# Kernel optimization log

Hardware: AMD Instinct MI355X
Metric: run time of the kernel (lower is better)

## Reference

```python
import jax, jax.numpy as jnp
import numpy as np

D_MODEL = 768
NUM_HEADS = 12
D_HEAD = D_MODEL // NUM_HEADS
LN_EPS = 1e-5


def layer_norm(x, w, b):
    m = jnp.mean(x, axis=-1, keepdims=True)
    v = jnp.mean(jnp.square(x - m), axis=-1, keepdims=True)
    return (x - m) * jax.lax.rsqrt(v + LN_EPS) * w + b


def setup_inputs() -> dict:
    key = jax.random.key(0)
    ks = jax.random.split(key, 10)
    B, P, NQ, D = 16, 197, 8, D_MODEL
    s = 1.0 / np.sqrt(D)
    return {
        "q_x": jax.random.normal(ks[0], (1, NQ, D), jnp.float32),
        "kv_x": jax.random.normal(ks[1], (B, P, D), jnp.float32),
        "pair_pos_embedding": jax.random.normal(ks[2], (2 * P, D), jnp.float32) * 0.02,
        "q_w": jax.random.normal(ks[3], (D, D), jnp.float32) * s,
        "q_b": jnp.zeros((D,), jnp.float32),
        "kv_w": jax.random.normal(ks[4], (D, D), jnp.float32) * s,
        "kv_b": jnp.zeros((D,), jnp.float32),
        "out_w": jax.random.normal(ks[5], (D, D), jnp.float32) * s,
        "out_b": jnp.zeros((D,), jnp.float32),
        "lnq_w": jnp.ones((D,), jnp.float32),
        "lnq_b": jnp.zeros((D,), jnp.float32),
        "lnkv_w": jnp.ones((D,), jnp.float32),
        "lnkv_b": jnp.zeros((D,), jnp.float32),
    }


def reference(q_x, kv_x, pair_pos_embedding, q_w, q_b, kv_w, kv_b,
              out_w, out_b, lnq_w, lnq_b, lnkv_w, lnkv_b):
    H, dh = NUM_HEADS, D_HEAD
    scale = dh ** -0.5
    _, NQ, D = q_x.shape
    B, P, _ = kv_x.shape

    # q path: Linear -> LN -> split heads -> [1, H, NQ, dh]
    q = layer_norm(q_x @ q_w.T + q_b, lnq_w, lnq_b)
    q = q.reshape(1, NQ, H, dh).transpose(0, 2, 1, 3)  # [1,H,NQ,dh]

    # kv path: Linear -> LN -> split heads -> [B, H, P, dh]
    kv = layer_norm(kv_x @ kv_w.T + kv_b, lnkv_w, lnkv_b)
    kv = kv.reshape(B, P, H, dh).transpose(0, 2, 1, 3)  # [B,H,P,dh]

    # pairwise expansion: kv_concat[i*B+j] = cat(kv[i], kv[j]) along token dim
    kv_rep = jnp.repeat(kv, B, axis=0)          # [B^2,H,P,dh] (repeat_interleave)
    kv_til = jnp.tile(kv, (B, 1, 1, 1))         # [B^2,H,P,dh]
    kv_cat = jnp.concatenate([kv_rep, kv_til], axis=2)  # [B^2,H,2P,dh]

    # positional bias: [2P, D] -> [1, H, 2P, dh]
    pos = pair_pos_embedding.reshape(1, 2 * P, H, dh).transpose(0, 2, 1, 3)
    kv_cat = kv_cat + pos

    scores = jnp.einsum('bhqd,bhpd->bhqp', jnp.broadcast_to(q, (B * B, H, NQ, dh)), kv_cat) * scale
    attn = jax.nn.softmax(scores, axis=-1)      # [B^2,H,NQ,2P]

    v1 = jnp.einsum('bhqp,bhpd->bhqd', attn[..., :P], kv_cat[:, :, :P, :])
    v2 = jnp.einsum('bhqp,bhpd->bhqd', attn[..., P:], kv_cat[:, :, P:, :])
    values = (v1 - v2).transpose(0, 2, 1, 3).reshape(B * B, NQ, D)
    return values @ out_w.T + out_b
```

## Files before the change

kernel.cpp:

```cpp
#include <hip/hip_runtime.h>
#include <hip/hip_bf16.h>
#include <math.h>

#define D_MODEL 768
#define NHEADS  12
#define DHEAD   64
#define NQR     8
#define BB      16
#define PP      197
#define NPAIR   256
#define MKV     (BB*PP)
#define LN_EPSF 1e-5f
#define SCALEF  0.125f

#define KTOT  2304
#define KSPLIT 3
#define KPER  (KTOT/KSPLIT)
#define MPAD  3200
#define BM 128
#define BN 128
#define BK 64

#define CH0   100
#define CH1   97
#define CHMAX 100

typedef __attribute__((ext_vector_type(8))) short short8v;
typedef __attribute__((ext_vector_type(4))) float float4v;

__device__ __forceinline__ void gload16(const void* g, void* l){
  __builtin_amdgcn_global_load_lds(
      (const __attribute__((address_space(1))) unsigned int*)g,
      (__attribute__((address_space(3))) unsigned int*)l, 16, 0, 0);
}

__device__ __forceinline__ float lane_bcast(float v, int src){
  return __int_as_float(__builtin_amdgcn_readlane(__float_as_int(v), src));
}

__global__ __launch_bounds__(192) void prep_kernel(
    const float* __restrict__ kvx, const float* __restrict__ kvw,
    __hip_bfloat16* __restrict__ Ab, __hip_bfloat16* __restrict__ Wb,
    const float* __restrict__ qx, const float* __restrict__ qw,
    float* __restrict__ qy)
{
  __shared__ float xs[NQR*D_MODEL];
  int b = blockIdx.x, t = threadIdx.x;
  if (b < MPAD + D_MODEL){
    const float* X; __hip_bfloat16* Y; int valid, mode, m;
    if (b < MPAD){ X = kvx; Y = Ab; valid = MKV;     mode = 0; m = b; }
    else         { X = kvw; Y = Wb; valid = D_MODEL; mode = 1; m = b - MPAD; }
    int k = t*4;
    float4 v = (m < valid) ? *(const float4*)&X[(size_t)m*D_MODEL + k]
                           : make_float4(0.f,0.f,0.f,0.f);
    float xsv[4] = {v.x, v.y, v.z, v.w};
    unsigned short hu[4], lu[4];
    #pragma unroll
    for (int i = 0; i < 4; i++){
      __hip_bfloat16 h = __float2bfloat16(xsv[i]);
      float hf = __bfloat162float(h);
      __hip_bfloat16 l = __float2bfloat16(xsv[i] - hf);
      hu[i] = *(unsigned short*)&h;
      lu[i] = *(unsigned short*)&l;
    }
    ushort4 hv = {hu[0], hu[1], hu[2], hu[3]};
    ushort4 lv = {lu[0], lu[1], lu[2], lu[3]};
    ushort4* row = (ushort4*)(Y + (size_t)m*KTOT);
    int s = k >> 2;
    if (mode == 0){ row[s] = hv; row[s+192] = hv; row[s+384] = lv; }
    else          { row[s] = hv; row[s+192] = lv; row[s+384] = hv; }
    return;
  }
  int b2 = b - (MPAD + D_MODEL);
  for (int e = t*4; e < NQR*D_MODEL; e += 768)
    *(float4*)&xs[e] = *(const float4*)&qx[e];
  __syncthreads();
  int col = t >> 5, lane = t & 31;
  int c = b2*6 + col;
  const float* wr = qw + (size_t)c*D_MODEL;
  float acc[NQR] = {};
  for (int k = lane*4; k < D_MODEL; k += 128){
    float4 w4 = *(const float4*)&wr[k];
    #pragma unroll
    for (int q = 0; q < NQR; q++){
      float4 x4 = *(const float4*)&xs[q*D_MODEL + k];
      acc[q] += x4.x*w4.x + x4.y*w4.y + x4.z*w4.z + x4.w*w4.w;
    }
  }
  #pragma unroll
  for (int q = 0; q < NQR; q++){
    float a = acc[q];
    for (int off = 16; off >= 1; off >>= 1) a += __shfl_xor(a, off, 32);
    if (lane == 0) qy[q*D_MODEL + c] = a;
  }
}

__global__ __launch_bounds__(256) void gemm_mfma_kernel(
    const __hip_bfloat16* __restrict__ Ab, const __hip_bfloat16* __restrict__ Wb,
    float* __restrict__ Cp)
{
  __shared__ __hip_bfloat16 As[BM*BK];
  __shared__ __hip_bfloat16 Bs[BN*BK];
  int tid = threadIdx.x;
  int wave = tid >> 6, lane = tid & 63;
  int m0 = blockIdx.x*BM, n0 = blockIdx.y*BN, kt = blockIdx.z;
  int wr = wave >> 1, wc = wave & 1;

  float4v acc[4][4];
  #pragma unroll
  for (int i = 0; i < 4; i++)
    #pragma unroll
    for (int j = 0; j < 4; j++)
      acc[i][j] = (float4v){0.f, 0.f, 0.f, 0.f};

  int sbase = wave*256;
  for (int st = 0; st < KPER/BK; ++st){
    int k0 = kt*KPER + st*BK;
    __syncthreads();
    #pragma unroll
    for (int i = 0; i < 4; i++){
      int s  = sbase + i*64 + lane;
      int r  = s >> 3, kg = s & 7;
      int kgg = kg ^ (r & 7);
      gload16(Ab + (size_t)(m0 + r)*KTOT + k0 + kgg*8, (char*)As + (size_t)s*16);
      gload16(Wb + (size_t)(n0 + r)*KTOT + k0 + kgg*8, (char*)Bs + (size_t)s*16);
    }
    __syncthreads();
    #pragma unroll
    for (int ks = 0; ks < 2; ks++){
      int kq = ks*4 + (lane >> 4);
      short8v af[4], bf[4];
      #pragma unroll
      for (int t = 0; t < 4; t++){
        int ar = wr*64 + t*16 + (lane & 15);
        int as_ = ar*8 + (kq ^ (ar & 7));
        af[t] = *(const short8v*)((const char*)As + (size_t)as_*16);
        int br = wc*64 + t*16 + (lane & 15);
        int bs_ = br*8 + (kq ^ (br & 7));
        bf[t] = *(const short8v*)((const char*)Bs + (size_t)bs_*16);
      }
      #pragma unroll
      for (int i = 0; i < 4; i++)
        #pragma unroll
        for (int j = 0; j < 4; j++)
          acc[i][j] = __builtin_amdgcn_mfma_f32_16x16x32_bf16(af[i], bf[j], acc[i][j], 0, 0, 0);
    }
  }

  float* C = Cp + (size_t)kt*MKV*D_MODEL;
  #pragma unroll
  for (int i = 0; i < 4; i++){
    int mb = m0 + wr*64 + i*16 + ((lane >> 4) << 2);
    #pragma unroll
    for (int j = 0; j < 4; j++){
      int n = n0 + wc*64 + j*16 + (lane & 15);
      #pragma unroll
      for (int r = 0; r < 4; r++){
        int m = mb + r;
        if (m < MKV) C[(size_t)m*D_MODEL + n] = acc[i][j][r];
      }
    }
  }
}

__global__ __launch_bounds__(256) void ln_all_kernel(
    const float* __restrict__ C0, const float* __restrict__ C1,
    const float* __restrict__ C2, const float* __restrict__ kv_b,
    const float* __restrict__ lnkv_w, const float* __restrict__ lnkv_b,
    float* __restrict__ kv_ln,
    const float* __restrict__ q_y, const float* __restrict__ q_b,
    const float* __restrict__ lnq_w, const float* __restrict__ lnq_b,
    float* __restrict__ q_ln)
{
  __shared__ float red[256], red2[256];
  int b = blockIdx.x, tid = threadIdx.x;
  const float *xa, *xb, *xc, *bias, *lw, *lb; float* outp; bool three;
  if (b < MKV){
    xa = C0 + (size_t)b*D_MODEL; xb = C1 + (size_t)b*D_MODEL;
    xc = C2 + (size_t)b*D_MODEL;
    bias = kv_b; lw = lnkv_w; lb = lnkv_b;
    outp = kv_ln + (size_t)b*D_MODEL; three = true;
  } else {
    int r = b - MKV;
    xa = q_y + (size_t)r*D_MODEL; xb = xa; xc = xa;
    bias = q_b; lw = lnq_w; lb = lnq_b;
    outp = q_ln + (size_t)r*D_MODEL; three = false;
  }
  float x0 = xa[tid      ] + (three ? xb[tid      ] + xc[tid      ] : 0.f) + bias[tid      ];
  float x1 = xa[tid + 256] + (three ? xb[tid + 256] + xc[tid + 256] : 0.f) + bias[tid + 256];
  float x2 = xa[tid + 512] + (three ? xb[tid + 512] + xc[tid + 512] : 0.f) + bias[tid + 512];
  red[tid] = x0 + x1 + x2; red2[tid] = x0*x0 + x1*x1 + x2*x2;
  __syncthreads();
  for (int st = 128; st > 0; st >>= 1){
    if (tid < st){ red[tid] += red[tid+st]; red2[tid] += red2[tid+st]; }
    __syncthreads();
  }
  float mean = red[0]*(1.f/768.f);
  float var  = red2[0]*(1.f/768.f) - mean*mean;
  float inv  = rsqrtf(var + LN_EPSF);
  outp[tid      ] = (x0-mean)*inv*lw[tid      ] + lb[tid      ];
  outp[tid + 256] = (x1-mean)*inv*lw[tid + 256] + lb[tid + 256];
  outp[tid + 512] = (x2-mean)*inv*lw[tid + 512] + lb[tid + 512];
}

__global__ __launch_bounds__(256) void rank_proj_kernel(
    const float* __restrict__ kv_ln, const float* __restrict__ q_ln,
    const float* __restrict__ ppe, const float* __restrict__ ow,
    float* __restrict__ z1O, float* __restrict__ z2O,
    float* __restrict__ p1, float* __restrict__ p2)
{
  __shared__ float A[CHMAX*65];
  __shared__ float Us[NQR*64];
  int r = blockIdx.x, h = blockIdx.y, half = blockIdx.z;
  int tid = threadIdx.x;
  int wave = tid >> 6, lane = tid & 63;
  int qa = 2*wave, qb = qa + 1;
  const float* qrowA = q_ln + (size_t)qa*D_MODEL + h*64;
  const float* qrowB = q_ln + (size_t)qb*D_MODEL + h*64;

  float ua = 0.f, ub = 0.f;
  float za = 0.f, zb = 0.f;

  for (int c = 0; c < 2; c++){
    int p0 = c ? CH0 : 0;
    int np = c ? CH1 : CH0;
    __syncthreads();
    for (int e = tid; e < np*16; e += 256){
      int p = e >> 4, dq = (e & 15) << 2;
      float4 a = *(const float4*)&kv_ln[((size_t)(r*PP + p0 + p))*D_MODEL + h*64 + dq];
      float4 b = *(const float4*)&ppe[((size_t)(half*PP + p0 + p))*D_MODEL + h*64 + dq];
      float* rw = &A[p*65 + dq];
      rw[0] = a.x + b.x; rw[1] = a.y + b.y;
      rw[2] = a.z + b.z; rw[3] = a.w + b.w;
    }
    __syncthreads();

    int p1v = lane + 64;
    bool v1 = p1v < np;
    int p1c = v1 ? p1v : 0;
    float s0a = 0.f, s0b = 0.f, s1a = 0.f, s1b = 0.f;
    for (int d = 0; d < 64; d++){
      float qva = qrowA[d];
      float qvb = qrowB[d];
      float a0 = A[lane*65 + d];
      float a1 = A[p1c*65 + d];
      s0a += qva*a0; s1a += qva*a1;
      s0b += qvb*a0; s1b += qvb*a1;
    }
    float e0a = __expf(s0a*SCALEF);
    float e0b = __expf(s0b*SCALEF);
    float e1a = v1 ? __expf(s1a*SCALEF) : 0.f;
    float e1b = v1 ? __expf(s1b*SCALEF) : 0.f;
    za += e0a + e1a;
    zb += e0b + e1b;

    for (int p = 0; p < 64; p++){
      float av = A[p*65 + lane];
      ua += lane_bcast(e0a, p) * av;
      ub += lane_bcast(e0b, p) * av;
    }
    for (int p = 64; p < np; p++){
      float av = A[p*65 + lane];
      ua += lane_bcast(e1a, p - 64) * av;
      ub += lane_bcast(e1b, p - 64) * av;
    }
  }

  for (int off = 32; off >= 1; off >>= 1){
    za += __shfl_xor(za, off);
    zb += __shfl_xor(zb, off);
  }
  float* zO = half ? z2O : z1O;
  if (lane == 0){
    zO[(r*NHEADS + h)*NQR + qa] = za;
    zO[(r*NHEADS + h)*NQR + qb] = zb;
  }
  Us[qa*64 + lane] = ua;
  Us[qb*64 + lane] = ub;
  __syncthreads();

  float acc[NQR][3];
  #pragma unroll
  for (int m = 0; m < NQR; m++){ acc[m][0]=0.f; acc[m][1]=0.f; acc[m][2]=0.f; }
  const float* owh = ow + h*64;
  for (int d4 = 0; d4 < 64; d4 += 4){
    float4 w0 = *(const float4*)&owh[(size_t)(tid      )*D_MODEL + d4];
    float4 w1 = *(const float4*)&owh[(size_t)(tid + 256)*D_MODEL + d4];
    float4 w2 = *(const float4*)&owh[(size_t)(tid + 512)*D_MODEL + d4];
    #pragma unroll
    for (int m = 0; m < NQR; m++){
      float4 u = *(const float4*)&Us[m*64 + d4];
      acc[m][0] += u.x*w0.x + u.y*w0.y + u.z*w0.z + u.w*w0.w;
      acc[m][1] += u.x*w1.x + u.y*w1.y + u.z*w1.z + u.w*w1.w;
      acc[m][2] += u.x*w2.x + u.y*w2.y + u.z*w2.z + u.w*w2.w;
    }
  }
  float* P = half ? p2 : p1;
  #pragma unroll
  for (int m = 0; m < NQR; m++){
    size_t obase = (((size_t)r*NHEADS + h)*NQR + m)*D_MODEL;
    #pragma unroll
    for (int j = 0; j < 3; j++)
      P[obase + tid + 256*j] = acc[m][j];
  }
}

__global__ __launch_bounds__(192) void combine_out_kernel(
    const float* __restrict__ z1, const float* __restrict__ z2,
    const float* __restrict__ p1, const float* __restrict__ p2,
    const float* __restrict__ out_b, float* __restrict__ out)
{
  __shared__ float cs[4][NHEADS];
  int i = blockIdx.x, q = blockIdx.y, jq = blockIdx.z;
  int j0 = jq*4;
  int tid = threadIdx.x;
  if (tid < 4*NHEADS){
    int j = tid / NHEADS, h = tid % NHEADS;
    int ii = (i*NHEADS + h)*NQR + q;
    int jj = ((j0 + j)*NHEADS + h)*NQR + q;
    cs[j][h] = 1.f / (z1[ii] + z2[jj]);
  }
  __syncthreads();

  int n4 = tid*4;
  float4 bv = *(const float4*)&out_b[n4];
  float4 acc[4];
  #pragma unroll
  for (int j = 0; j < 4; j++) acc[j] = bv;

  #pragma unroll
  for (int h = 0; h < NHEADS; h++){
    float4 a = *(const float4*)&p1[(((size_t)i*NHEADS + h)*NQR + q)*D_MODEL + n4];
    #pragma unroll
    for (int j = 0; j < 4; j++){
      float4 b = *(const float4*)&p2[(((size_t)(j0+j)*NHEADS + h)*NQR + q)*D_MODEL + n4];
      float c = cs[j][h];
      acc[j].x += c*(a.x - b.x);
      acc[j].y += c*(a.y - b.y);
      acc[j].z += c*(a.z - b.z);
      acc[j].w += c*(a.w - b.w);
    }
  }
  #pragma unroll
  for (int j = 0; j < 4; j++){
    int pair = i*BB + j0 + j;
    *(float4*)&out[((size_t)(pair*NQR + q))*D_MODEL + n4] = acc[j];
  }
}

extern "C" void kernel_launch(void* const* d_in, const int* in_sizes, int n_in,
                              void* d_out, int out_size, void* d_ws, size_t ws_size,
                              hipStream_t stream)
{
  const float* q_x    = (const float*)d_in[0];
  const float* kv_x   = (const float*)d_in[1];
  const float* ppe    = (const float*)d_in[2];
  const float* q_w    = (const float*)d_in[3];
  const float* q_b    = (const float*)d_in[4];
  const float* kv_w   = (const float*)d_in[5];
  const float* kv_b   = (const float*)d_in[6];
  const float* out_w  = (const float*)d_in[7];
  const float* out_b  = (const float*)d_in[8];
  const float* lnq_w  = (const float*)d_in[9];
  const float* lnq_b  = (const float*)d_in[10];
  const float* lnkv_w = (const float*)d_in[11];
  const float* lnkv_b = (const float*)d_in[12];
  float* out = (float*)d_out;

  float* ws    = (float*)d_ws;
  float* q_y   = ws;
  float* q_ln  = q_y  + NQR*D_MODEL;
  float* Abuf_f = q_ln + NQR*D_MODEL;
  float* Wbuf_f = Abuf_f + (size_t)MPAD*KTOT/2;
  float* C0    = Wbuf_f + (size_t)D_MODEL*KTOT/2;
  float* C1    = C0 + (size_t)MKV*D_MODEL;
  float* C2    = C1 + (size_t)MKV*D_MODEL;

  __hip_bfloat16* Abuf = (__hip_bfloat16*)Abuf_f;
  __hip_bfloat16* Wbuf = (__hip_bfloat16*)Wbuf_f;

  float* kv_ln = Abuf_f;
  float* z1    = Wbuf_f;
  float* z2    = z1 + BB*NHEADS*NQR;
  float* p1    = C0;
  float* p2    = p1 + (size_t)BB*NHEADS*NQR*D_MODEL;

  prep_kernel<<<MPAD + D_MODEL + 128, 192, 0, stream>>>(
      kv_x, kv_w, Abuf, Wbuf, q_x, q_w, q_y);

  gemm_mfma_kernel<<<dim3(MPAD/BM, D_MODEL/BN, KSPLIT), 256, 0, stream>>>(
      Abuf, Wbuf, C0);

  ln_all_kernel<<<MKV + NQR, 256, 0, stream>>>(
      C0, C1, C2, kv_b, lnkv_w, lnkv_b, kv_ln,
      q_y, q_b, lnq_w, lnq_b, q_ln);

  rank_proj_kernel<<<dim3(BB, NHEADS, 2), 256, 0, stream>>>(
      kv_ln, q_ln, ppe, out_w, z1, z2, p1, p2);

  combine_out_kernel<<<dim3(BB, NQR, 4), 192, 0, stream>>>(
      z1, z2, p1, p2, out_b, out);
}
```

Measured before the change: 173.0 us.

## Split rank projection into per-chunk attention kernel plus merge/projection kernel

```diff
diff --git a/kernel.cpp b/kernel.cpp
--- a/kernel.cpp
+++ b/kernel.cpp
@@ -24,6 +24,7 @@
 #define CH0   100
 #define CH1   97
 #define CHMAX 100
+#define NIDX  (BB*NHEADS*2*NQR)
 
 typedef __attribute__((ext_vector_type(8))) short short8v;
 typedef __attribute__((ext_vector_type(4))) float float4v;
@@ -203,80 +204,95 @@
   outp[tid + 512] = (x2-mean)*inv*lw[tid + 512] + lb[tid + 512];
 }
 
-__global__ __launch_bounds__(256) void rank_proj_kernel(
+__global__ __launch_bounds__(256) void rank_chunk_kernel(
     const float* __restrict__ kv_ln, const float* __restrict__ q_ln,
-    const float* __restrict__ ppe, const float* __restrict__ ow,
-    float* __restrict__ z1O, float* __restrict__ z2O,
-    float* __restrict__ p1, float* __restrict__ p2)
+    const float* __restrict__ ppe,
+    float* __restrict__ zC, float* __restrict__ UC)
 {
   __shared__ float A[CHMAX*65];
-  __shared__ float Us[NQR*64];
-  int r = blockIdx.x, h = blockIdx.y, half = blockIdx.z;
+  int r = blockIdx.x, h = blockIdx.y;
+  int half = blockIdx.z >> 1, c = blockIdx.z & 1;
+  int p0 = c ? CH0 : 0;
+  int np = c ? CH1 : CH0;
   int tid = threadIdx.x;
   int wave = tid >> 6, lane = tid & 63;
   int qa = 2*wave, qb = qa + 1;
   const float* qrowA = q_ln + (size_t)qa*D_MODEL + h*64;
   const float* qrowB = q_ln + (size_t)qb*D_MODEL + h*64;
 
+  for (int e = tid; e < np*16; e += 256){
+    int p = e >> 4, dq = (e & 15) << 2;
+    float4 a = *(const float4*)&kv_ln[((size_t)(r*PP + p0 + p))*D_MODEL + h*64 + dq];
+    float4 b = *(const float4*)&ppe[((size_t)(half*PP + p0 + p))*D_MODEL + h*64 + dq];
+    float* rw = &A[p*65 + dq];
+    rw[0] = a.x + b.x; rw[1] = a.y + b.y;
+    rw[2] = a.z + b.z; rw[3] = a.w + b.w;
+  }
+  __syncthreads();
+
+  int p1v = lane + 64;
+  bool v1 = p1v < np;
+  int p1c = v1 ? p1v : 0;
+  float s0a = 0.f, s0b = 0.f, s1a = 0.f, s1b = 0.f;
+  for (int d = 0; d < 64; d++){
+    float qva = qrowA[d];
+    float qvb = qrowB[d];
+    float a0 = A[lane*65 + d];
+    float a1 = A[p1c*65 + d];
+    s0a += qva*a0; s1a += qva*a1;
+    s0b += qvb*a0; s1b += qvb*a1;
+  }
+  float e0a = __expf(s0a*SCALEF);
+  float e0b = __expf(s0b*SCALEF);
+  float e1a = v1 ? __expf(s1a*SCALEF) : 0.f;
+  float e1b = v1 ? __expf(s1b*SCALEF) : 0.f;
+  float za = e0a + e1a;
+  float zb = e0b + e1b;
+
   float ua = 0.f, ub = 0.f;
-  float za = 0.f, zb = 0.f;
-
-  for (int c = 0; c < 2; c++){
-    int p0 = c ? CH0 : 0;
-    int np = c ? CH1 : CH0;
-    __syncthreads();
-    for (int e = tid; e < np*16; e += 256){
-      int p = e >> 4, dq = (e & 15) << 2;
-      float4 a = *(const float4*)&kv_ln[((size_t)(r*PP + p0 + p))*D_MODEL + h*64 + dq];
-      float4 b = *(const float4*)&ppe[((size_t)(half*PP + p0 + p))*D_MODEL + h*64 + dq];
-      float* rw = &A[p*65 + dq];
-      rw[0] = a.x + b.x; rw[1] = a.y + b.y;
-      rw[2] = a.z + b.z; rw[3] = a.w + b.w;
-    }
-    __syncthreads();
-
-    int p1v = lane + 64;
-    bool v1 = p1v < np;
-    int p1c = v1 ? p1v : 0;
-    float s0a = 0.f, s0b = 0.f, s1a = 0.f, s1b = 0.f;
-    for (int d = 0; d < 64; d++){
-      float qva = qrowA[d];
-      float qvb = qrowB[d];
-      float a0 = A[lane*65 + d];
-      float a1 = A[p1c*65 + d];
-      s0a += qva*a0; s1a += qva*a1;
-      s0b += qvb*a0; s1b += qvb*a1;
-    }
-    float e0a = __expf(s0a*SCALEF);
-    float e0b = __expf(s0b*SCALEF);
-    float e1a = v1 ? __expf(s1a*SCALEF) : 0.f;
-    float e1b = v1 ? __expf(s1b*SCALEF) : 0.f;
-    za += e0a + e1a;
-    zb += e0b + e1b;
-
-    for (int p = 0; p < 64; p++){
-      float av = A[p*65 + lane];
-      ua += lane_bcast(e0a, p) * av;
-      ub += lane_bcast(e0b, p) * av;
-    }
-    for (int p = 64; p < np; p++){
-      float av = A[p*65 + lane];
-      ua += lane_bcast(e1a, p - 64) * av;
-      ub += lane_bcast(e1b, p - 64) * av;
-    }
+  for (int p = 0; p < 64; p++){
+    float av = A[p*65 + lane];
+    ua += lane_bcast(e0a, p) * av;
+    ub += lane_bcast(e0b, p) * av;
+  }
+  for (int p = 64; p < np; p++){
+    float av = A[p*65 + lane];
+    ua += lane_bcast(e1a, p - 64) * av;
+    ub += lane_bcast(e1b, p - 64) * av;
   }
 
   for (int off = 32; off >= 1; off >>= 1){
     za += __shfl_xor(za, off);
     zb += __shfl_xor(zb, off);
   }
-  float* zO = half ? z2O : z1O;
+  int idxa = ((r*NHEADS + h)*2 + half)*NQR + qa;
+  int idxb = idxa + 1;
   if (lane == 0){
-    zO[(r*NHEADS + h)*NQR + qa] = za;
-    zO[(r*NHEADS + h)*NQR + qb] = zb;
-  }
-  Us[qa*64 + lane] = ua;
-  Us[qb*64 + lane] = ub;
+    zC[c*NIDX + idxa] = za;
+    zC[c*NIDX + idxb] = zb;
+  }
+  UC[((size_t)(c*NIDX + idxa))*64 + lane] = ua;
+  UC[((size_t)(c*NIDX + idxb))*64 + lane] = ub;
+}
+
+__global__ __launch_bounds__(256) void merge_proj_kernel(
+    const float* __restrict__ zC, const float* __restrict__ UC,
+    const float* __restrict__ ow,
+    float* __restrict__ z1O, float* __restrict__ z2O,
+    float* __restrict__ p1, float* __restrict__ p2)
+{
+  __shared__ float Us[NQR*64];
+  int r = blockIdx.x, h = blockIdx.y, half = blockIdx.z;
+  int tid = threadIdx.x;
+  int base = ((r*NHEADS + h)*2 + half)*NQR;
+
+  for (int e = tid; e < NQR*64; e += 256)
+    Us[e] = UC[(size_t)base*64 + e] + UC[((size_t)NIDX + base)*64 + e];
+  if (tid < NQR){
+    float z = zC[base + tid] + zC[NIDX + base + tid];
+    float* zO = half ? z2O : z1O;
+    zO[(r*NHEADS + h)*NQR + tid] = z;
+  }
   __syncthreads();
 
   float acc[NQR][3];
@@ -380,7 +396,9 @@
   __hip_bfloat16* Wbuf = (__hip_bfloat16*)Wbuf_f;
 
   float* kv_ln = Abuf_f;
-  float* z1    = Wbuf_f;
+  float* zC    = Wbuf_f;
+  float* UC    = zC + 2*NIDX;
+  float* z1    = UC + (size_t)2*NIDX*64;
   float* z2    = z1 + BB*NHEADS*NQR;
   float* p1    = C0;
   float* p2    = p1 + (size_t)BB*NHEADS*NQR*D_MODEL;
@@ -395,8 +413,11 @@
       C0, C1, C2, kv_b, lnkv_w, lnkv_b, kv_ln,
       q_y, q_b, lnq_w, lnq_b, q_ln);
 
-  rank_proj_kernel<<<dim3(BB, NHEADS, 2), 256, 0, stream>>>(
-      kv_ln, q_ln, ppe, out_w, z1, z2, p1, p2);
+  rank_chunk_kernel<<<dim3(BB, NHEADS, 4), 256, 0, stream>>>(
+      kv_ln, q_ln, ppe, zC, UC);
+
+  merge_proj_kernel<<<dim3(BB, NHEADS, 2), 256, 0, stream>>>(
+      zC, UC, out_w, z1, z2, p1, p2);
 
   combine_out_kernel<<<dim3(BB, NQR, 4), 192, 0, stream>>>(
       z1, z2, p1, p2, out_b, out);
```

Measured after the change: 172.7 us. About the same (-0.1%).
